# Kernel tuning notes

Hardware: AMD Instinct MI355X
Metric: run time of the kernel (lower is better)

The kernel has to match this reference:

```python
import jax, jax.numpy as jnp
import numpy as np

N = 80000        # nodes
E = 1280000      # edges (avg degree 16)
D_IN, H1, H2, D_OUT = 64, 64, 64, 64


def _glorot(key, fan_in, fan_out):
    s = np.sqrt(6.0 / (fan_in + fan_out)).astype(np.float32)
    return jax.random.uniform(key, (fan_in, fan_out), jnp.float32, -s, s)


def setup_inputs() -> dict:
    key = jax.random.key(0)
    ks = jax.random.split(key, 5)
    X = jax.random.normal(ks[0], (N, D_IN), jnp.float32)
    edge_index = jax.random.randint(ks[1], (2, E), 0, N, dtype=jnp.int32).astype(jnp.int64)
    W1 = _glorot(ks[2], D_IN, H1)
    W2 = _glorot(ks[3], H1, H2)
    W3 = _glorot(ks[4], H2, D_OUT)
    b1 = jnp.zeros((H1,), jnp.float32)
    b2 = jnp.zeros((H2,), jnp.float32)
    b3 = jnp.zeros((D_OUT,), jnp.float32)
    return {"X": X, "edge_index": edge_index,
            "W1": W1, "b1": b1, "W2": W2, "b2": b2, "W3": W3, "b3": b3}


def _gcn_conv(x, W, b, src, dst, n):
    """PyG GCNConv: symmetric-normalized mean over A + I, then linear + bias.
    x' = D^{-1/2} (A + I) D^{-1/2} (x W) + b, deg counts self-loops."""
    x = x @ W                                   # [N, F_out]
    # in-degree including self loop (edge weights are 1)
    deg = jnp.ones((n,), x.dtype).at[dst].add(1.0)
    dinv = jax.lax.rsqrt(deg)                   # deg >= 1 always
    coef = dinv[src] * dinv[dst]                # [E]
    msg = x[src] * coef[:, None]                # [E, F_out] gather
    agg = jnp.zeros_like(x).at[dst].add(msg)    # scatter-add to targets
    agg = agg + x * (dinv * dinv)[:, None]      # self-loop contribution
    return agg + b


def reference(X, edge_index, W1, b1, W2, b2, W3, b3):
    src, dst = edge_index[0], edge_index[1]
    n = X.shape[0]
    h = jax.nn.relu(_gcn_conv(X, W1, b1, src, dst, n))
    h = jax.nn.relu(_gcn_conv(h, W2, b2, src, dst, n))
    out = _gcn_conv(h, W3, b3, src, dst, n)     # no activation on last layer
    return out
```

## Files before the change

kernel.cpp:

```cpp
#include <hip/hip_runtime.h>
#include <hip/hip_fp16.h>

#define NN 80000
#define NE 1280000
#define F  64
#define BSH 9
#define NB  157
#define CAP 12288
#define EPB 5120
#define EPT 10
#define PBLK (NE / EPB)

typedef _Float16 half_t;
typedef _Float16 half8 __attribute__((ext_vector_type(8)));
typedef float f32x4 __attribute__((ext_vector_type(4)));
typedef unsigned int uint_t;

__device__ __forceinline__ float2 h2f2(uint_t u) {
    __half2 h = *(__half2*)&u;
    return __half22float2(h);
}

__device__ __forceinline__ int ld_src(const int* __restrict__ idx, int e, int is64) {
    return is64 ? idx[2 * e] : idx[e];
}
__device__ __forceinline__ int ld_dst(const int* __restrict__ idx, int e, int is64) {
    return is64 ? idx[2 * NE + 2 * e] : idx[NE + e];
}

__global__ __launch_bounds__(512) void partition_kernel(
        const int* __restrict__ idx,
        int* __restrict__ bcur, int* __restrict__ ebuf) {
    __shared__ int cnt[NB];
    __shared__ int lbase[NB];
    __shared__ int gbase[NB];
    __shared__ int lds_val[EPB];
    __shared__ int lds_gaddr[EPB];
    __shared__ int is64_s;
    int tid = threadIdx.x;
    if (tid == 0) is64_s = 1;
    if (tid < NB) cnt[tid] = 0;
    __syncthreads();
    if (idx[2 * tid + 1] != 0) is64_s = 0;
    __syncthreads();
    int is64 = is64_s;
    int e0 = blockIdx.x * EPB;
    int val[EPT], br[EPT];
    #pragma unroll
    for (int j = 0; j < EPT; ++j) {
        int e = e0 + j * 512 + tid;
        int s = ld_src(idx, e, is64);
        int d = ld_dst(idx, e, is64);
        int b = d >> BSH;
        val[j] = ((d & ((1 << BSH) - 1)) << 17) | s;
        int r = atomicAdd(&cnt[b], 1);
        br[j] = (b << 13) | r;
    }
    __syncthreads();
    if (tid < 64) {
        int carry = 0;
        for (int base = 0; base < NB; base += 64) {
            int i2 = base + tid;
            int v = (i2 < NB) ? cnt[i2] : 0;
            int incl = v;
            #pragma unroll
            for (int d2 = 1; d2 < 64; d2 <<= 1) {
                int t = __shfl_up(incl, d2, 64);
                if (tid >= d2) incl += t;
            }
            if (i2 < NB) lbase[i2] = carry + incl - v;
            carry += __shfl(incl, 63);
        }
    } else if (tid - 64 < NB) {
        int b = tid - 64;
        gbase[b] = atomicAdd(&bcur[b], cnt[b]);
    }
    __syncthreads();
    #pragma unroll
    for (int j = 0; j < EPT; ++j) {
        int b = br[j] >> 13, r = br[j] & 8191;
        int slot = lbase[b] + r;
        int g = gbase[b] + r;
        lds_val[slot]   = val[j];
        lds_gaddr[slot] = (g < CAP) ? (b * CAP + g) : -1;
    }
    __syncthreads();
    for (int i = tid; i < EPB; i += 512) {
        int a = lds_gaddr[i];
        if (a >= 0) ebuf[a] = lds_val[i];
    }
}

__global__ __launch_bounds__(1024) void bucket_sort_kernel(
        const int* __restrict__ bcur, const int* __restrict__ ebuf,
        const float* __restrict__ X,
        int* __restrict__ edata, int* __restrict__ row_ptr,
        float* __restrict__ dinv, half_t* __restrict__ y0) {
    __shared__ int cnt[512];
    __shared__ int off[512];
    __shared__ int lds_out[CAP];
    __shared__ int ebase_s;
    int b = blockIdx.x, tid = threadIdx.x;
    if (tid < 512) cnt[tid] = 0;
    if (tid < 64) {
        int carry = 0;
        for (int base = 0; base < NB; base += 64) {
            int i2 = base + tid;
            int v = (i2 < NB) ? min(bcur[i2], CAP) : 0;
            int incl = v;
            #pragma unroll
            for (int d2 = 1; d2 < 64; d2 <<= 1) {
                int t = __shfl_up(incl, d2, 64);
                if (tid >= d2) incl += t;
            }
            if (i2 == b) ebase_s = carry + incl - v;
            carry += __shfl(incl, 63);
        }
    }
    __syncthreads();
    int bcnt = min(bcur[b], CAP);
    int ebase = ebase_s;
    const int* src = ebuf + b * CAP;
    for (int i = tid; i < bcnt; i += 1024)
        atomicAdd(&cnt[src[i] >> 17], 1);
    __syncthreads();
    if (tid < 64) {
        int carry = 0;
        #pragma unroll
        for (int base = 0; base < 512; base += 64) {
            int v = cnt[base + tid];
            int incl = v;
            #pragma unroll
            for (int d2 = 1; d2 < 64; d2 <<= 1) {
                int t = __shfl_up(incl, d2, 64);
                if (tid >= d2) incl += t;
            }
            off[base + tid] = carry + incl - v;
            carry += __shfl(incl, 63);
        }
    }
    __syncthreads();
    int n0 = b << BSH;
    if (tid < 512) {
        int n = n0 + tid;
        if (n < NN) {
            row_ptr[n] = ebase + off[tid];
            dinv[n] = rsqrtf((float)cnt[tid] + 1.f);
        } else if (n == NN) {
            row_ptr[NN] = ebase + off[tid];
        }
    }
    __syncthreads();
    for (int i = tid; i < bcnt; i += 1024) {
        int w = src[i];
        int pos = atomicAdd(&off[w >> 17], 1);
        lds_out[pos] = w & 0x1FFFF;
    }
    __syncthreads();
    for (int i = tid; i < bcnt; i += 1024)
        edata[ebase + i] = lds_out[i];
    for (int i = tid; i < (512 << 4); i += 1024) {
        int r = i >> 4, qq = i & 15;
        int n = n0 + r;
        if (n < NN) {
            float c = rsqrtf((float)cnt[r] + 1.f);
            float4 v = ((const float4*)(X + (size_t)n * F))[qq];
            half_t h[4] = { (half_t)(v.x * c), (half_t)(v.y * c),
                            (half_t)(v.z * c), (half_t)(v.w * c) };
            ((uint2*)(y0 + (size_t)n * F))[qq] = *(uint2*)h;
        }
    }
}

__device__ __forceinline__ uint4 ldrow(const half_t* __restrict__ y, int s, int fl) {
    return ((const uint4*)(y + (size_t)s * F))[fl];
}

__device__ __forceinline__ void acc8(float* a, const uint4& u, float m) {
    float2 f0 = h2f2(u.x), f1 = h2f2(u.y);
    float2 f2 = h2f2(u.z), f3 = h2f2(u.w);
    a[0] = fmaf(m, f0.x, a[0]); a[1] = fmaf(m, f0.y, a[1]);
    a[2] = fmaf(m, f1.x, a[2]); a[3] = fmaf(m, f1.y, a[3]);
    a[4] = fmaf(m, f2.x, a[4]); a[5] = fmaf(m, f2.y, a[5]);
    a[6] = fmaf(m, f3.x, a[6]); a[7] = fmaf(m, f3.y, a[7]);
}

__device__ __forceinline__ void batch32(float* a, const half_t* __restrict__ y,
        const int* __restrict__ edata, int p, int sub, int fl) {
    int s[4];
    #pragma unroll
    for (int j = 0; j < 4; ++j) s[j] = edata[p + j * 8 + sub];
    uint4 u[4];
    #pragma unroll
    for (int j = 0; j < 4; ++j) u[j] = ldrow(y, s[j], fl);
    #pragma unroll
    for (int j = 0; j < 4; ++j) acc8(a, u[j], 1.f);
}

template <int RELU, int LAST>
__global__ __launch_bounds__(512, 4) void fused_layer(
        const half_t* __restrict__ y,
        const int* __restrict__ edata, const int* __restrict__ row_ptr,
        const float* __restrict__ dinv,
        const float* __restrict__ W, const float* __restrict__ bias,
        half_t* __restrict__ out_h, float* __restrict__ out_f32) {
    __shared__ __align__(16) half_t Wt[64][72];
    __shared__ __align__(16) half_t xt[64][72];
    int tid = threadIdx.x;
    for (int i = tid; i < 4096; i += 512) {
        int k = i >> 6, n2 = i & 63;
        Wt[n2][k] = (half_t)W[i];
    }
    int wv = tid >> 6, lane = tid & 63;
    int sub = lane >> 3;
    int fl  = lane & 7;
    int n0 = blockIdx.x * 64;
    int rbase = wv * 8;
    int rp = row_ptr[n0 + rbase + (lane < 9 ? lane : 8)];
    #pragma unroll 1
    for (int i = 0; i < 8; i += 2) {
        int nA = n0 + rbase + i;
        int pA0 = __shfl(rp, i), pA1 = __shfl(rp, i + 1), pB1 = __shfl(rp, i + 2);
        int pB0 = pA1;
        uint4 usA = ldrow(y, nA, fl);
        uint4 usB = ldrow(y, nA + 1, fl);
        float aA[8], aB[8];
        #pragma unroll
        for (int j = 0; j < 8; ++j) { aA[j] = 0.f; aB[j] = 0.f; }
        int pA = pA0, pB = pB0;
        while (pA + 32 <= pA1) { batch32(aA, y, edata, pA, sub, fl); pA += 32; }
        while (pB + 32 <= pB1) { batch32(aB, y, edata, pB, sub, fl); pB += 32; }
        int sA[4], sB[4]; float mA[4], mB[4];
        #pragma unroll
        for (int j = 0; j < 4; ++j) {
            int qA = pA + j * 8 + sub;
            int cA = qA < pA1 ? qA : pA1 - 1;  cA = cA > 0 ? cA : 0;
            sA[j] = edata[cA];  mA[j] = (qA < pA1) ? 1.f : 0.f;
            int qB = pB + j * 8 + sub;
            int cB = qB < pB1 ? qB : pB1 - 1;  cB = cB > 0 ? cB : 0;
            sB[j] = edata[cB];  mB[j] = (qB < pB1) ? 1.f : 0.f;
        }
        uint4 uA[4], uB[4];
        #pragma unroll
        for (int j = 0; j < 4; ++j) { uA[j] = ldrow(y, sA[j], fl);
                                      uB[j] = ldrow(y, sB[j], fl); }
        #pragma unroll
        for (int j = 0; j < 4; ++j) { acc8(aA, uA[j], mA[j]);
                                      acc8(aB, uB[j], mB[j]); }
        #pragma unroll
        for (int j = 0; j < 8; ++j) {
            aA[j] += __shfl_down(aA[j], 32);
            aA[j] += __shfl_down(aA[j], 16);
            aA[j] += __shfl_down(aA[j], 8);
            aB[j] += __shfl_down(aB[j], 32);
            aB[j] += __shfl_down(aB[j], 16);
            aB[j] += __shfl_down(aB[j], 8);
        }
        if (sub == 0) {
            float dvA = rsqrtf((float)(pA1 - pA0) + 1.f);
            float2 s0 = h2f2(usA.x), s1 = h2f2(usA.y), s2 = h2f2(usA.z), s3 = h2f2(usA.w);
            half_t h[8] = {
                (half_t)(dvA * (aA[0] + s0.x)), (half_t)(dvA * (aA[1] + s0.y)),
                (half_t)(dvA * (aA[2] + s1.x)), (half_t)(dvA * (aA[3] + s1.y)),
                (half_t)(dvA * (aA[4] + s2.x)), (half_t)(dvA * (aA[5] + s2.y)),
                (half_t)(dvA * (aA[6] + s3.x)), (half_t)(dvA * (aA[7] + s3.y)) };
            *(uint4*)&xt[rbase + i][fl * 8] = *(uint4*)h;
            float dvB = rsqrtf((float)(pB1 - pB0) + 1.f);
            float2 t0 = h2f2(usB.x), t1 = h2f2(usB.y), t2 = h2f2(usB.z), t3 = h2f2(usB.w);
            half_t g[8] = {
                (half_t)(dvB * (aB[0] + t0.x)), (half_t)(dvB * (aB[1] + t0.y)),
                (half_t)(dvB * (aB[2] + t1.x)), (half_t)(dvB * (aB[3] + t1.y)),
                (half_t)(dvB * (aB[4] + t2.x)), (half_t)(dvB * (aB[5] + t2.y)),
                (half_t)(dvB * (aB[6] + t3.x)), (half_t)(dvB * (aB[7] + t3.y)) };
            *(uint4*)&xt[rbase + i + 1][fl * 8] = *(uint4*)g;
        }
    }
    __syncthreads();
    int m = lane & 15, q = lane >> 4;
    int rt = (wv & 3) * 16;
    int ct0 = (wv >> 2) * 2;
    const half_t* arow = &xt[rt + m][q * 8];
    half8 A0 = *(const half8*)arow;
    half8 A1 = *(const half8*)(arow + 32);
    float dvr[4];
    if (!LAST) {
        #pragma unroll
        for (int r = 0; r < 4; ++r) dvr[r] = dinv[n0 + rt + q * 4 + r];
    }
    #pragma unroll
    for (int c2 = 0; c2 < 2; ++c2) {
        int ct = (ct0 + c2) * 16;
        const half_t* brow = &Wt[ct + m][q * 8];
        half8 B0 = *(const half8*)brow;
        half8 B1 = *(const half8*)(brow + 32);
        f32x4 c = {0.f, 0.f, 0.f, 0.f};
        c = __builtin_amdgcn_mfma_f32_16x16x32_f16(A0, B0, c, 0, 0, 0);
        c = __builtin_amdgcn_mfma_f32_16x16x32_f16(A1, B1, c, 0, 0, 0);
        float bv = bias[ct + m];
        #pragma unroll
        for (int r = 0; r < 4; ++r) {
            int row = n0 + rt + q * 4 + r;
            float v = c[r] + bv;
            if (RELU) v = fmaxf(v, 0.f);
            int col = ct + m;
            if (LAST) out_f32[(size_t)row * F + col] = v;
            else      out_h[(size_t)row * F + col] = (half_t)(v * dvr[r]);
        }
    }
}

extern "C" void kernel_launch(void* const* d_in, const int* in_sizes, int n_in,
                              void* d_out, int out_size, void* d_ws, size_t ws_size,
                              hipStream_t stream) {
    const float* X  = (const float*)d_in[0];
    const int*  idx = (const int*)d_in[1];
    const float* W1 = (const float*)d_in[2];
    const float* b1 = (const float*)d_in[3];
    const float* W2 = (const float*)d_in[4];
    const float* b2 = (const float*)d_in[5];
    const float* W3 = (const float*)d_in[6];
    const float* b3 = (const float*)d_in[7];
    float* out = (float*)d_out;

    char* ws = (char*)d_ws;
    int*    bcur    = (int*)(ws + 256);
    int*    row_ptr = (int*)(ws + 1024);
    float*  dinv    = (float*)(ws + 321280);
    int*    edata   = (int*)(ws + 641536);
    half_t* ybufA   = (half_t*)(ws + 5761536);
    half_t* ybufB   = (half_t*)(ws + 16001536);
    int*    ebuf    = (int*)(ws + 26241536);

    hipMemsetAsync(bcur, 0, NB * sizeof(int), stream);
    partition_kernel<<<PBLK, 512, 0, stream>>>(idx, bcur, ebuf);
    bucket_sort_kernel<<<NB, 1024, 0, stream>>>(bcur, ebuf, X, edata, row_ptr, dinv, ybufA);

    const int fBlocks = NN / 64;

    fused_layer<1, 0><<<fBlocks, 512, 0, stream>>>(ybufA, edata, row_ptr, dinv, W1, b1, ybufB, nullptr);
    fused_layer<1, 0><<<fBlocks, 512, 0, stream>>>(ybufB, edata, row_ptr, dinv, W2, b2, ybufA, nullptr);
    fused_layer<0, 1><<<fBlocks, 512, 0, stream>>>(ybufA, edata, row_ptr, dinv, W3, b3, nullptr, out);
}
```

Baseline: 221.1 us.

## Assign one node per 8-lane group in aggregation and defer weight staging

```diff
diff --git a/kernel.cpp b/kernel.cpp
--- a/kernel.cpp
+++ b/kernel.cpp
@@ -185,20 +185,8 @@
     a[6] = fmaf(m, f3.x, a[6]); a[7] = fmaf(m, f3.y, a[7]);
 }
 
-__device__ __forceinline__ void batch32(float* a, const half_t* __restrict__ y,
-        const int* __restrict__ edata, int p, int sub, int fl) {
-    int s[4];
-    #pragma unroll
-    for (int j = 0; j < 4; ++j) s[j] = edata[p + j * 8 + sub];
-    uint4 u[4];
-    #pragma unroll
-    for (int j = 0; j < 4; ++j) u[j] = ldrow(y, s[j], fl);
-    #pragma unroll
-    for (int j = 0; j < 4; ++j) acc8(a, u[j], 1.f);
-}
-
 template <int RELU, int LAST>
-__global__ __launch_bounds__(512, 4) void fused_layer(
+__global__ __launch_bounds__(512, 6) void fused_layer(
         const half_t* __restrict__ y,
         const int* __restrict__ edata, const int* __restrict__ row_ptr,
         const float* __restrict__ dinv,
@@ -207,90 +195,70 @@
     __shared__ __align__(16) half_t Wt[64][72];
     __shared__ __align__(16) half_t xt[64][72];
     int tid = threadIdx.x;
-    for (int i = tid; i < 4096; i += 512) {
-        int k = i >> 6, n2 = i & 63;
-        Wt[n2][k] = (half_t)W[i];
-    }
+    float wreg[8];
+    #pragma unroll
+    for (int i = 0; i < 8; ++i) wreg[i] = W[tid + i * 512];
     int wv = tid >> 6, lane = tid & 63;
-    int sub = lane >> 3;
-    int fl  = lane & 7;
+    int g = lane >> 3;
+    int q = lane & 7;
+    int gbase = lane & 56;
     int n0 = blockIdx.x * 64;
     int rbase = wv * 8;
-    int rp = row_ptr[n0 + rbase + (lane < 9 ? lane : 8)];
+    int node = n0 + rbase + g;
+    int p0 = row_ptr[node], p1 = row_ptr[node + 1];
+    int deg = p1 - p0;
+    int dmax = deg;
+    dmax = max(dmax, __shfl_xor(dmax, 8));
+    dmax = max(dmax, __shfl_xor(dmax, 16));
+    dmax = max(dmax, __shfl_xor(dmax, 32));
+    uint4 us = ldrow(y, node, q);
+    float a[8];
+    {
+        float2 f0 = h2f2(us.x), f1 = h2f2(us.y);
+        float2 f2 = h2f2(us.z), f3 = h2f2(us.w);
+        a[0] = f0.x; a[1] = f0.y; a[2] = f1.x; a[3] = f1.y;
+        a[4] = f2.x; a[5] = f2.y; a[6] = f3.x; a[7] = f3.y;
+    }
     #pragma unroll 1
-    for (int i = 0; i < 8; i += 2) {
-        int nA = n0 + rbase + i;
-        int pA0 = __shfl(rp, i), pA1 = __shfl(rp, i + 1), pB1 = __shfl(rp, i + 2);
-        int pB0 = pA1;
-        uint4 usA = ldrow(y, nA, fl);
-        uint4 usB = ldrow(y, nA + 1, fl);
-        float aA[8], aB[8];
+    for (int k8 = 0; k8 < dmax; k8 += 8) {
+        int ei = p0 + k8 + q;
+        ei = min(ei, p1 - 1); ei = max(ei, 0);
+        int e = edata[ei];
         #pragma unroll
-        for (int j = 0; j < 8; ++j) { aA[j] = 0.f; aB[j] = 0.f; }
-        int pA = pA0, pB = pB0;
-        while (pA + 32 <= pA1) { batch32(aA, y, edata, pA, sub, fl); pA += 32; }
-        while (pB + 32 <= pB1) { batch32(aB, y, edata, pB, sub, fl); pB += 32; }
-        int sA[4], sB[4]; float mA[4], mB[4];
-        #pragma unroll
-        for (int j = 0; j < 4; ++j) {
-            int qA = pA + j * 8 + sub;
-            int cA = qA < pA1 ? qA : pA1 - 1;  cA = cA > 0 ? cA : 0;
-            sA[j] = edata[cA];  mA[j] = (qA < pA1) ? 1.f : 0.f;
-            int qB = pB + j * 8 + sub;
-            int cB = qB < pB1 ? qB : pB1 - 1;  cB = cB > 0 ? cB : 0;
-            sB[j] = edata[cB];  mB[j] = (qB < pB1) ? 1.f : 0.f;
-        }
-        uint4 uA[4], uB[4];
-        #pragma unroll
-        for (int j = 0; j < 4; ++j) { uA[j] = ldrow(y, sA[j], fl);
-                                      uB[j] = ldrow(y, sB[j], fl); }
-        #pragma unroll
-        for (int j = 0; j < 4; ++j) { acc8(aA, uA[j], mA[j]);
-                                      acc8(aB, uB[j], mB[j]); }
-        #pragma unroll
-        for (int j = 0; j < 8; ++j) {
-            aA[j] += __shfl_down(aA[j], 32);
-            aA[j] += __shfl_down(aA[j], 16);
-            aA[j] += __shfl_down(aA[j], 8);
-            aB[j] += __shfl_down(aB[j], 32);
-            aB[j] += __shfl_down(aB[j], 16);
-            aB[j] += __shfl_down(aB[j], 8);
-        }
-        if (sub == 0) {
-            float dvA = rsqrtf((float)(pA1 - pA0) + 1.f);
-            float2 s0 = h2f2(usA.x), s1 = h2f2(usA.y), s2 = h2f2(usA.z), s3 = h2f2(usA.w);
-            half_t h[8] = {
-                (half_t)(dvA * (aA[0] + s0.x)), (half_t)(dvA * (aA[1] + s0.y)),
-                (half_t)(dvA * (aA[2] + s1.x)), (half_t)(dvA * (aA[3] + s1.y)),
-                (half_t)(dvA * (aA[4] + s2.x)), (half_t)(dvA * (aA[5] + s2.y)),
-                (half_t)(dvA * (aA[6] + s3.x)), (half_t)(dvA * (aA[7] + s3.y)) };
-            *(uint4*)&xt[rbase + i][fl * 8] = *(uint4*)h;
-            float dvB = rsqrtf((float)(pB1 - pB0) + 1.f);
-            float2 t0 = h2f2(usB.x), t1 = h2f2(usB.y), t2 = h2f2(usB.z), t3 = h2f2(usB.w);
-            half_t g[8] = {
-                (half_t)(dvB * (aB[0] + t0.x)), (half_t)(dvB * (aB[1] + t0.y)),
-                (half_t)(dvB * (aB[2] + t1.x)), (half_t)(dvB * (aB[3] + t1.y)),
-                (half_t)(dvB * (aB[4] + t2.x)), (half_t)(dvB * (aB[5] + t2.y)),
-                (half_t)(dvB * (aB[6] + t3.x)), (half_t)(dvB * (aB[7] + t3.y)) };
-            *(uint4*)&xt[rbase + i + 1][fl * 8] = *(uint4*)g;
-        }
-    }
-    __syncthreads();
-    int m = lane & 15, q = lane >> 4;
+        for (int k = 0; k < 8; ++k) {
+            int s = __shfl(e, gbase | k);
+            uint4 u = ldrow(y, s, q);
+            float m = (k8 + k < deg) ? 1.f : 0.f;
+            acc8(a, u, m);
+        }
+    }
+    float dv = rsqrtf((float)deg + 1.f);
+    half_t h[8] = { (half_t)(dv * a[0]), (half_t)(dv * a[1]),
+                    (half_t)(dv * a[2]), (half_t)(dv * a[3]),
+                    (half_t)(dv * a[4]), (half_t)(dv * a[5]),
+                    (half_t)(dv * a[6]), (half_t)(dv * a[7]) };
+    *(uint4*)&xt[rbase + g][q * 8] = *(uint4*)h;
+    #pragma unroll
+    for (int i = 0; i < 8; ++i) {
+        int i2 = tid + i * 512;
+        Wt[i2 & 63][i2 >> 6] = (half_t)wreg[i];
+    }
+    __syncthreads();
+    int m = lane & 15, q4 = lane >> 4;
     int rt = (wv & 3) * 16;
     int ct0 = (wv >> 2) * 2;
-    const half_t* arow = &xt[rt + m][q * 8];
+    const half_t* arow = &xt[rt + m][q4 * 8];
     half8 A0 = *(const half8*)arow;
     half8 A1 = *(const half8*)(arow + 32);
     float dvr[4];
     if (!LAST) {
         #pragma unroll
-        for (int r = 0; r < 4; ++r) dvr[r] = dinv[n0 + rt + q * 4 + r];
+        for (int r = 0; r < 4; ++r) dvr[r] = dinv[n0 + rt + q4 * 4 + r];
     }
     #pragma unroll
     for (int c2 = 0; c2 < 2; ++c2) {
         int ct = (ct0 + c2) * 16;
-        const half_t* brow = &Wt[ct + m][q * 8];
+        const half_t* brow = &Wt[ct + m][q4 * 8];
         half8 B0 = *(const half8*)brow;
         half8 B1 = *(const half8*)(brow + 32);
         f32x4 c = {0.f, 0.f, 0.f, 0.f};
@@ -299,7 +267,7 @@
         float bv = bias[ct + m];
         #pragma unroll
         for (int r = 0; r < 4; ++r) {
-            int row = n0 + rt + q * 4 + r;
+            int row = n0 + rt + q4 * 4 + r;
             float v = c[r] + bv;
             if (RELU) v = fmaxf(v, 0.f);
             int col = ct + m;
```

Result: slower. 233.8 us (+5.8%).
